# Performance work log

Hardware: AMD Instinct MI355X
Metric: run time of the kernel (lower is better)

## Reference

```python
import jax, jax.numpy as jnp
import numpy as np

EMBED = 1024
HEADS = 16
HD = EMBED // HEADS
SCALE_BASE = 512
OFFSET = 0

def _dup_interleave(m):
    # [T, half] -> [T, 2*half], each column repeated twice interleaved
    return jnp.repeat(m, 2, axis=-1)

def _rotate_every_two(x):
    x1 = x[..., ::2]
    x2 = x[..., 1::2]
    return jnp.stack([-x2, x1], axis=-1).reshape(x.shape)

def _xpos(x, offset, downscale):
    # x: [B, H, T, D]; torchscale XPOS
    T = x.shape[2]
    half = HD // 2
    scale_vec = (jnp.arange(0, HD, 2, dtype=jnp.float32) + 0.4 * HD) / (1.4 * HD)  # [half]
    min_pos = -(T + offset) // 2
    power = jnp.arange(min_pos, min_pos + T, dtype=jnp.float32) / SCALE_BASE  # [T]
    scale = scale_vec[None, :] ** power[:, None]  # [T, half]
    inv_freq = 1.0 / (10000.0 ** (jnp.arange(half, dtype=jnp.float32) / half))
    ang = jnp.arange(T, dtype=jnp.float32)[:, None] * inv_freq[None, :]  # [T, half]
    sin, cos = jnp.sin(ang), jnp.cos(ang)
    if downscale:
        scale = 1.0 / scale
    sin_s = _dup_interleave(sin * scale)  # [T, D]
    cos_s = _dup_interleave(cos * scale)  # [T, D]
    return x * cos_s + _rotate_every_two(x) * sin_s

def setup_inputs() -> dict:
    rng = jax.random.key(0)
    ks = jax.random.split(rng, 8)
    B, T, C = 2, 2048, EMBED
    s = 1.0 / np.sqrt(C)
    return {
        "query": jax.random.normal(ks[0], (B, T, C), jnp.float32),
        "key": jax.random.normal(ks[1], (B, T, C), jnp.float32),
        "value": jax.random.normal(ks[2], (B, T, C), jnp.float32),
        "key_padding_mask": jnp.zeros((B, T), jnp.bool_),
        "Wq": jax.random.normal(ks[3], (C, C), jnp.float32) * s,
        "bq": jnp.zeros((C,), jnp.float32),
        "Wk": jax.random.normal(ks[4], (C, C), jnp.float32) * s,
        "bk": jnp.zeros((C,), jnp.float32),
        "Wv": jax.random.normal(ks[5], (C, C), jnp.float32) * s,
        "bv": jnp.zeros((C,), jnp.float32),
        "Wo": jax.random.normal(ks[6], (C, C), jnp.float32) * s,
        "bo": jnp.zeros((C,), jnp.float32),
    }

def reference(query, key, value, key_padding_mask, Wq, bq, Wk, bk, Wv, bv, Wo, bo):
    B, T, C = query.shape
    def split(x):  # [B,T,C] -> [B,H,T,D]
        return x.reshape(B, T, HEADS, HD).transpose(0, 2, 1, 3)
    q = split(query @ Wq + bq)
    k = split(key @ Wk + bk)
    v = split(value @ Wv + bv)
    k = _xpos(k, 0, True)
    q = _xpos(q, OFFSET, False)
    scores = jnp.einsum('bhtd,bhsd->bhts', q * (HD ** -0.5), k)
    scores = jnp.where(key_padding_mask[:, None, None, :], -jnp.inf, scores)
    probs = jax.nn.softmax(scores.astype(jnp.float32), axis=-1).astype(scores.dtype)
    out = jnp.einsum('bhts,bhsd->bhtd', probs, v)
    out = out.transpose(0, 2, 1, 3).reshape(B, T, C)
    return out @ Wo + bo
```

## Files before the change

kernel.cpp:

```cpp
#include <hip/hip_runtime.h>
#include <math.h>


typedef _Float16 half4v __attribute__((ext_vector_type(4)));
typedef _Float16 half8v __attribute__((ext_vector_type(8)));
typedef float floatx4 __attribute__((ext_vector_type(4)));

#define GLOAD_LDS16(g, l)                                          \
    __builtin_amdgcn_global_load_lds(                              \
        (const __attribute__((address_space(1))) void*)(g),        \
        (__attribute__((address_space(3))) void*)(l), 16, 0, 0)

__global__ __launch_bounds__(256) void convert_x_kernel(
    const float* __restrict__ q, const float* __restrict__ k,
    const float* __restrict__ v, _Float16* __restrict__ oq,
    _Float16* __restrict__ ok, _Float16* __restrict__ ov)
{
    const int z = blockIdx.y;
    const float* src = (z == 0) ? q : (z == 1) ? k : v;
    _Float16* dst = (z == 0) ? oq : (z == 1) ? ok : ov;
    const size_t i = ((size_t)blockIdx.x * 256 + threadIdx.x) * 4;
    const float4 f = *(const float4*)(src + i);
    half4v h = {(_Float16)f.x, (_Float16)f.y, (_Float16)f.z, (_Float16)f.w};
    *(half4v*)(dst + i) = h;
}

__global__ __launch_bounds__(256) void convert_wt_kernel(
    const float* __restrict__ Wq, const float* __restrict__ Wk,
    const float* __restrict__ Wv, const float* __restrict__ Wo,
    _Float16* __restrict__ Wt)
{
    __shared__ float t[64][65];
    const int z = blockIdx.z;
    const float* W = (z == 0) ? Wq : (z == 1) ? Wk : (z == 2) ? Wv : Wo;
    _Float16* out = Wt + (size_t)z * 1048576;
    const int kt = blockIdx.y << 6;
    const int nb = blockIdx.x << 6;
    const int tid = threadIdx.x;

#pragma unroll
    for (int rep = 0; rep < 4; ++rep) {
        const int row = rep * 16 + (tid >> 4);
        const int col = (tid & 15) << 2;
        const float4 f = *(const float4*)(W + (size_t)(kt + row) * 1024 + nb + col);
        t[row][col + 0] = f.x; t[row][col + 1] = f.y;
        t[row][col + 2] = f.z; t[row][col + 3] = f.w;
    }
    __syncthreads();
#pragma unroll
    for (int rep = 0; rep < 2; ++rep) {
        const int n = rep * 32 + (tid >> 3);
        const int k8 = (tid & 7) << 3;
        half8v h;
#pragma unroll
        for (int j = 0; j < 8; ++j) h[j] = (_Float16)t[k8 + j][n];
        *(half8v*)(out + (size_t)(nb + n) * 1024 + kt + k8) = h;
    }
}

__global__ __launch_bounds__(256) void xpos_tables_kernel(
    float* __restrict__ csQ, float* __restrict__ snQ,
    float* __restrict__ csK, float* __restrict__ snK)
{
    const int idx = blockIdx.x * 256 + threadIdx.x;
    const int t = idx >> 5, j = idx & 31;
    const float invf = exp2f(-(float)j * 0.41524101186092029f);
    const float ang = (float)t * invf;
    const float sn = __sinf(ang), cs = __cosf(ang);
    const float lsv = log2f((2.0f * j + 25.6f) * (1.0f / 89.6f));
    const float pw = ((float)t - 1024.0f) * (1.0f / 512.0f);
    const float scQ = exp2f(pw * lsv) * 0.125f * 1.44269504088896341f;
    const float scK = exp2f(-pw * lsv);
    const int o = (t << 6) + 2 * j;
    csQ[o] = cs * scQ; csQ[o + 1] = cs * scQ;
    snQ[o] = -sn * scQ; snQ[o + 1] = sn * scQ;
    csK[o] = cs * scK; csK[o + 1] = cs * scK;
    snK[o] = -sn * scK; snK[o + 1] = sn * scK;
}

__global__ __launch_bounds__(256) void gemm_qkv_kernel(
    const _Float16* __restrict__ Xq, const _Float16* __restrict__ Xk,
    const _Float16* __restrict__ Xv, const _Float16* __restrict__ Wt,
    const float* __restrict__ bq, const float* __restrict__ bk,
    const float* __restrict__ bv,
    const float* __restrict__ csQ, const float* __restrict__ snQ,
    const float* __restrict__ csK, const float* __restrict__ snK,
    _Float16* __restrict__ Qr, _Float16* __restrict__ Kr,
    _Float16* __restrict__ Vt)
{
    __shared__ _Float16 smem[16384];

    const int zone  = blockIdx.x >> 3;
    const int ncol0 = (blockIdx.x & 7) << 7;
    const _Float16* Ab = (zone == 0) ? Xq : (zone == 1) ? Xk : Xv;
    const _Float16* Bb = Wt + (size_t)zone * 1048576;
    const float* bias = (zone == 0) ? bq : (zone == 1) ? bk : bv;

    const int tid  = threadIdx.x;
    const int wave = tid >> 6;
    const int lane = tid & 63;
    const int l15  = lane & 15;
    const int q4   = lane >> 4;

    const int mBase = blockIdx.y << 7;

    const int c0 = tid, c1 = tid + 256;
    const int rA0 = c0 >> 2, g0 = (c0 & 3) ^ ((rA0 >> 1) & 3);
    const int rA1 = c1 >> 2, g1 = (c1 & 3) ^ ((rA1 >> 1) & 3);
    const _Float16* gA0 = Ab + (size_t)(mBase + rA0) * 1024 + g0 * 8;
    const _Float16* gA1 = Ab + (size_t)(mBase + rA1) * 1024 + g1 * 8;
    const _Float16* gB0 = Bb + (size_t)(ncol0 + rA0) * 1024 + g0 * 8;
    const _Float16* gB1 = Bb + (size_t)(ncol0 + rA1) * 1024 + g1 * 8;

    const int mW = (wave >> 1) << 6;
    const int nW = (wave & 1) << 6;

    floatx4 acc[4][4];
#pragma unroll
    for (int i = 0; i < 4; ++i)
#pragma unroll
        for (int j = 0; j < 4; ++j) acc[i][j] = (floatx4){0.f, 0.f, 0.f, 0.f};

#define QKV_STAGE(k0, buf)                                         \
    do {                                                           \
        _Float16* sb = smem + (buf) * 8192;                        \
        GLOAD_LDS16(gA0 + (k0), sb + c0 * 8);                      \
        GLOAD_LDS16(gA1 + (k0), sb + c1 * 8);                      \
        GLOAD_LDS16(gB0 + (k0), sb + 4096 + c0 * 8);               \
        GLOAD_LDS16(gB1 + (k0), sb + 4096 + c1 * 8);               \
    } while (0)

    QKV_STAGE(0, 0);

    for (int it = 0; it < 32; ++it) {
        const int b = it & 1;
        __syncthreads();
        if (it < 31) QKV_STAGE((it + 1) << 5, b ^ 1);

        const _Float16* sb = smem + b * 8192;
        half8v af[4], bf[4];
#pragma unroll
        for (int mt = 0; mt < 4; ++mt) {
            const int r = mW + mt * 16 + l15;
            af[mt] = *(const half8v*)(sb + r * 32 + ((q4 ^ ((r >> 1) & 3)) << 3));
        }
#pragma unroll
        for (int nt = 0; nt < 4; ++nt) {
            const int r = nW + nt * 16 + l15;
            bf[nt] = *(const half8v*)(sb + 4096 + r * 32 + ((q4 ^ ((r >> 1) & 3)) << 3));
        }
#pragma unroll
        for (int mt = 0; mt < 4; ++mt)
#pragma unroll
            for (int nt = 0; nt < 4; ++nt)
                acc[mt][nt] = __builtin_amdgcn_mfma_f32_16x16x32_f16(
                    af[mt], bf[nt], acc[mt][nt], 0, 0, 0);
    }
#undef QKV_STAGE

    if (zone <= 1) {
        const float* csT = zone ? csK : csQ;
        const float* snT = zone ? snK : snQ;
        _Float16* dst = zone ? Kr : Qr;
#pragma unroll
        for (int nt = 0; nt < 4; ++nt) {
            const int col = ncol0 + nW + nt * 16 + l15;
            const int h = col >> 6, d = col & 63;
            const float bb = bias[col];
#pragma unroll
            for (int mt = 0; mt < 4; ++mt) {
#pragma unroll
                for (int reg = 0; reg < 4; ++reg) {
                    const int r = mBase + mW + mt * 16 + q4 * 4 + reg;
                    const int t = r & 2047, b = r >> 11;
                    const float x = acc[mt][nt][reg] + bb;
                    const float p = __shfl_xor(x, 1);
                    const int ti = (t << 6) + d;
                    const float o = csT[ti] * x + snT[ti] * p;
                    dst[(((size_t)(b * 16 + h) * 2048 + t) << 6) + d] = (_Float16)o;
                }
            }
        }
    } else {
#pragma unroll
        for (int nt = 0; nt < 4; ++nt) {
            const int col = ncol0 + nW + nt * 16 + l15;
            const int h = col >> 6, d = col & 63;
            const float bb = bias[col];
#pragma unroll
            for (int mt = 0; mt < 4; ++mt) {
                const int r0 = mBase + mW + mt * 16 + q4 * 4;
                const int t0 = r0 & 2047, b = r0 >> 11;
                half4v w = {(_Float16)(acc[mt][nt][0] + bb),
                            (_Float16)(acc[mt][nt][1] + bb),
                            (_Float16)(acc[mt][nt][2] + bb),
                            (_Float16)(acc[mt][nt][3] + bb)};
                *(half4v*)(Vt + ((size_t)(b * 16 + h) * 64 + d) * 2048 + t0) = w;
            }
        }
    }
}

__global__ __launch_bounds__(512) void gemm_out_kernel(
    const _Float16* __restrict__ Ar, const _Float16* __restrict__ Wt,
    const float* __restrict__ bo, float* __restrict__ Out)
{
    __shared__ _Float16 smem[16384];

    const _Float16* Bb = Wt + (size_t)3 * 1048576;
    const int tid  = threadIdx.x;
    const int wave = tid >> 6;
    const int lane = tid & 63;
    const int l15  = lane & 15;
    const int q4   = lane >> 4;

    const int mBase = blockIdx.y << 7;
    const int nBase = blockIdx.x << 7;

    const int rS = tid >> 2, gS = (tid & 3) ^ ((rS >> 1) & 3);
    const _Float16* gA = Ar + (size_t)(mBase + rS) * 1024 + gS * 8;
    const _Float16* gB = Bb + (size_t)(nBase + rS) * 1024 + gS * 8;

    const int mW = (wave >> 2) << 6;
    const int nW = (wave & 3) << 5;

    floatx4 acc[4][2];
#pragma unroll
    for (int i = 0; i < 4; ++i)
#pragma unroll
        for (int j = 0; j < 2; ++j) acc[i][j] = (floatx4){0.f, 0.f, 0.f, 0.f};

#define OUT_STAGE(k0, buf)                                         \
    do {                                                           \
        _Float16* sb = smem + (buf) * 8192;                        \
        GLOAD_LDS16(gA + (k0), sb + tid * 8);                      \
        GLOAD_LDS16(gB + (k0), sb + 4096 + tid * 8);               \
    } while (0)

    OUT_STAGE(0, 0);

    for (int it = 0; it < 32; ++it) {
        const int b = it & 1;
        __syncthreads();
        if (it < 31) OUT_STAGE((it + 1) << 5, b ^ 1);

        const _Float16* sb = smem + b * 8192;
        half8v af[4], bf[2];
#pragma unroll
        for (int mt = 0; mt < 4; ++mt) {
            const int r = mW + mt * 16 + l15;
            af[mt] = *(const half8v*)(sb + r * 32 + ((q4 ^ ((r >> 1) & 3)) << 3));
        }
#pragma unroll
        for (int nt = 0; nt < 2; ++nt) {
            const int r = nW + nt * 16 + l15;
            bf[nt] = *(const half8v*)(sb + 4096 + r * 32 + ((q4 ^ ((r >> 1) & 3)) << 3));
        }
#pragma unroll
        for (int mt = 0; mt < 4; ++mt)
#pragma unroll
            for (int nt = 0; nt < 2; ++nt)
                acc[mt][nt] = __builtin_amdgcn_mfma_f32_16x16x32_f16(
                    af[mt], bf[nt], acc[mt][nt], 0, 0, 0);
    }
#undef OUT_STAGE

#pragma unroll
    for (int nt = 0; nt < 2; ++nt) {
        const int col = nBase + nW + nt * 16 + l15;
        const float bb = bo[col];
#pragma unroll
        for (int mt = 0; mt < 4; ++mt) {
#pragma unroll
            for (int reg = 0; reg < 4; ++reg) {
                const int r = mBase + mW + mt * 16 + q4 * 4 + reg;
                Out[(size_t)r * 1024 + col] = acc[mt][nt][reg] + bb;
            }
        }
    }
}

__global__ __launch_bounds__(512, 4) void attn_mfma_kernel(
    const _Float16* __restrict__ Q, const _Float16* __restrict__ K,
    const _Float16* __restrict__ Vt, _Float16* __restrict__ Ar)
{
    __shared__ _Float16 Ks[2][4096];
    __shared__ _Float16 Vs[2][4096];
    __shared__ _Float16 Ps[8][1024];

    const int tid  = threadIdx.x;
    const int wave = tid >> 6;
    const int lane = tid & 63;
    const int l15  = lane & 15;
    const int q4   = lane >> 4;
    const int swz  = l15 & 7;

    const int bh    = blockIdx.y;
    const int qBase = blockIdx.x << 7;
    const _Float16* Qh = Q  + ((size_t)bh << 17);
    const _Float16* Kh = K  + ((size_t)bh << 17);
    const _Float16* Vh = Vt + ((size_t)bh << 17);

    const _Float16* qp =
        Qh + ((size_t)(qBase + wave * 16 + l15) << 6) + q4 * 8;
    const half8v qf0 = *(const half8v*)(qp);
    const half8v qf1 = *(const half8v*)(qp + 32);

    floatx4 O[4];
#pragma unroll
    for (int i = 0; i < 4; ++i) O[i] = (floatx4){0.f, 0.f, 0.f, 0.f};
    floatx4 l_acc = (floatx4){0.f, 0.f, 0.f, 0.f};
    float mneg = 64.0f;
    const half8v ones = {(_Float16)1, (_Float16)1, (_Float16)1, (_Float16)1,
                         (_Float16)1, (_Float16)1, (_Float16)1, (_Float16)1};

    const int sA = tid >> 3, gA = (tid & 7) ^ (sA & 7);

#define STAGE(S0, BUF)                                                        \
    do {                                                                      \
        GLOAD_LDS16(Kh + (size_t)((S0) + sA) * 64 + gA * 8, &Ks[BUF][tid * 8]);\
        GLOAD_LDS16(Vh + (size_t)sA * 2048 + (S0) + gA * 8, &Vs[BUF][tid * 8]);\
    } while (0)

    STAGE(0, 0);

    for (int ci = 0; ci < 32; ++ci) {
        const int b = ci & 1;
        __syncthreads();
        if (ci < 31) STAGE((ci + 1) << 6, b ^ 1);

        const floatx4 bias = (floatx4){mneg, mneg, mneg, mneg};
        floatx4 St[4];
        __builtin_amdgcn_s_setprio(1);
#pragma unroll
        for (int ti = 0; ti < 4; ++ti) {
            const _Float16* kb = &Ks[b][(ti * 16 + l15) << 6];
            const half8v kf0 = *(const half8v*)(kb + ((q4 ^ swz) << 3));
            const half8v kf1 = *(const half8v*)(kb + (((q4 ^ 4) ^ swz) << 3));
            floatx4 a = __builtin_amdgcn_mfma_f32_16x16x32_f16(
                kf0, qf0, bias, 0, 0, 0);
            St[ti] = __builtin_amdgcn_mfma_f32_16x16x32_f16(
                kf1, qf1, a, 0, 0, 0);
        }
        __builtin_amdgcn_s_setprio(0);

        float mx0 = fmaxf(fmaxf(St[0][0], St[0][1]), St[0][2]);
        float mx1 = fmaxf(fmaxf(St[0][3], St[1][0]), St[1][1]);
        float mx2 = fmaxf(fmaxf(St[1][2], St[1][3]), St[2][0]);
        float mx3 = fmaxf(fmaxf(St[2][1], St[2][2]), St[2][3]);
        float mx4 = fmaxf(fmaxf(St[3][0], St[3][1]), St[3][2]);
        float mx  = fmaxf(fmaxf(mx0, mx1), mx2);
        mx = fmaxf(fmaxf(mx, mx3), fmaxf(mx4, St[3][3]));

        if (__any(mx > 8.0f)) {
            mx = fmaxf(mx, __shfl_xor(mx, 16));
            mx = fmaxf(mx, __shfl_xor(mx, 32));
            const float dlt = fmaxf(mx, 0.0f);
            const float alpha = __builtin_amdgcn_exp2f(-dlt);
            mneg -= dlt;
#pragma unroll
            for (int ti = 0; ti < 4; ++ti)
#pragma unroll
                for (int reg = 0; reg < 4; ++reg) St[ti][reg] -= dlt;
            float ar[4];
#pragma unroll
            for (int reg = 0; reg < 4; ++reg)
                ar[reg] = __shfl(alpha, 20 * q4 + reg);
#pragma unroll
            for (int dt = 0; dt < 4; ++dt)
#pragma unroll
                for (int reg = 0; reg < 4; ++reg) O[dt][reg] *= ar[reg];
#pragma unroll
            for (int reg = 0; reg < 4; ++reg) l_acc[reg] *= ar[reg];
        }

#pragma unroll
        for (int ti = 0; ti < 4; ++ti)
#pragma unroll
            for (int reg = 0; reg < 4; ++reg)
                St[ti][reg] = __builtin_amdgcn_exp2f(St[ti][reg]);

        _Float16* pw = &Ps[wave][l15 << 6];
#pragma unroll
        for (int ti = 0; ti < 4; ++ti) {
            const int sg = 2 * ti + (q4 >> 1);
            half4v pv = {(_Float16)St[ti][0], (_Float16)St[ti][1],
                         (_Float16)St[ti][2], (_Float16)St[ti][3]};
            *(half4v*)(pw + ((sg ^ swz) << 3) + ((q4 & 1) << 2)) = pv;
        }

        const _Float16* pr = &Ps[wave][l15 << 6];
        const half8v pa0 = *(const half8v*)(pr + ((q4 ^ swz) << 3));
        const half8v pa1 = *(const half8v*)(pr + (((q4 ^ 4) ^ swz) << 3));
        __builtin_amdgcn_s_setprio(1);
        l_acc = __builtin_amdgcn_mfma_f32_16x16x32_f16(pa0, ones, l_acc, 0, 0, 0);
        l_acc = __builtin_amdgcn_mfma_f32_16x16x32_f16(pa1, ones, l_acc, 0, 0, 0);
#pragma unroll
        for (int dt = 0; dt < 4; ++dt) {
            const _Float16* vbp = &Vs[b][(dt * 16 + l15) << 6];
            const half8v vb0 = *(const half8v*)(vbp + ((q4 ^ swz) << 3));
            const half8v vb1 = *(const half8v*)(vbp + (((q4 ^ 4) ^ swz) << 3));
            O[dt] = __builtin_amdgcn_mfma_f32_16x16x32_f16(
                pa0, vb0, O[dt], 0, 0, 0);
            O[dt] = __builtin_amdgcn_mfma_f32_16x16x32_f16(
                pa1, vb1, O[dt], 0, 0, 0);
        }
        __builtin_amdgcn_s_setprio(0);
    }
#undef STAGE

    const int b_ = bh >> 4, h = bh & 15;
#pragma unroll
    for (int reg = 0; reg < 4; ++reg) {
        const float inv = 1.0f / l_acc[reg];
        const int t = qBase + wave * 16 + 4 * q4 + reg;
        _Float16* po = Ar + ((size_t)(b_ * 2048 + t)) * 1024 + h * 64 + l15;
#pragma unroll
        for (int dt = 0; dt < 4; ++dt)
            po[dt * 16] = (_Float16)(O[dt][reg] * inv);
    }
}

extern "C" void kernel_launch(void* const* d_in, const int* in_sizes, int n_in,
                              void* d_out, int out_size, void* d_ws, size_t ws_size,
                              hipStream_t stream) {
    const float* q  = (const float*)d_in[0];
    const float* k  = (const float*)d_in[1];
    const float* v  = (const float*)d_in[2];
    const float* Wq = (const float*)d_in[4];
    const float* bq = (const float*)d_in[5];
    const float* Wk = (const float*)d_in[6];
    const float* bk = (const float*)d_in[7];
    const float* Wv = (const float*)d_in[8];
    const float* bv = (const float*)d_in[9];
    const float* Wo = (const float*)d_in[10];
    const float* bo = (const float*)d_in[11];
    float* out = (float*)d_out;

    _Float16* Xqf = (_Float16*)d_ws;
    _Float16* Xkf = Xqf + (size_t)4194304;
    _Float16* Xvf = Xkf + (size_t)4194304;
    _Float16* Wt  = Xvf + (size_t)4194304;
    _Float16* Qr  = Wt  + (size_t)4194304;
    _Float16* Kr  = Qr  + (size_t)4194304;
    _Float16* Vt  = Kr  + (size_t)4194304;
    _Float16* Ar  = Vt  + (size_t)4194304;

    float* csQ = (float*)Ar;
    float* snQ = csQ + 131072;
    float* csK = snQ + 131072;
    float* snK = csK + 131072;

    dim3 blk(256, 1, 1);
    convert_x_kernel<<<dim3(4096, 3, 1), blk, 0, stream>>>(q, k, v, Xqf, Xkf, Xvf);
    convert_wt_kernel<<<dim3(16, 16, 4), blk, 0, stream>>>(Wq, Wk, Wv, Wo, Wt);
    xpos_tables_kernel<<<dim3(256, 1, 1), blk, 0, stream>>>(csQ, snQ, csK, snK);
    gemm_qkv_kernel<<<dim3(24, 32, 1), blk, 0, stream>>>(
        Xqf, Xkf, Xvf, Wt, bq, bk, bv, csQ, snQ, csK, snK, Qr, Kr, Vt);
    attn_mfma_kernel<<<dim3(16, 32, 1), dim3(512, 1, 1), 0, stream>>>(Qr, Kr, Vt, Ar);
    gemm_out_kernel<<<dim3(8, 32, 1), dim3(512, 1, 1), 0, stream>>>(Ar, Wt, bo, out);
}
```

Measured before the change: 246.1 us.

## Fuse prep kernels, XCD-aware block remap, smaller out-GEMM tiles, unroll attention loop

Merges the three preprocessing kernels (activation cast, weight transpose, xpos tables) into one launch to cut launch overhead. Remaps block indices in the QKV GEMM, attention and output GEMM so that blocks sharing operands land on the same XCD for better L2 reuse. The output GEMM tile shrinks from 128x128 to 128x64 to launch more blocks, which costs more reloads of A. The attention chunk loop is unrolled by two through a macro so the buffer index is a compile-time constant.

```diff
diff --git a/kernel.cpp b/kernel.cpp
--- a/kernel.cpp
+++ b/kernel.cpp
@@ -11,71 +11,70 @@
         (const __attribute__((address_space(1))) void*)(g),        \
         (__attribute__((address_space(3))) void*)(l), 16, 0, 0)
 
-__global__ __launch_bounds__(256) void convert_x_kernel(
+__global__ __launch_bounds__(256) void prep_kernel(
     const float* __restrict__ q, const float* __restrict__ k,
     const float* __restrict__ v, _Float16* __restrict__ oq,
-    _Float16* __restrict__ ok, _Float16* __restrict__ ov)
-{
-    const int z = blockIdx.y;
-    const float* src = (z == 0) ? q : (z == 1) ? k : v;
-    _Float16* dst = (z == 0) ? oq : (z == 1) ? ok : ov;
-    const size_t i = ((size_t)blockIdx.x * 256 + threadIdx.x) * 4;
-    const float4 f = *(const float4*)(src + i);
-    half4v h = {(_Float16)f.x, (_Float16)f.y, (_Float16)f.z, (_Float16)f.w};
-    *(half4v*)(dst + i) = h;
-}
-
-__global__ __launch_bounds__(256) void convert_wt_kernel(
+    _Float16* __restrict__ ok, _Float16* __restrict__ ov,
     const float* __restrict__ Wq, const float* __restrict__ Wk,
     const float* __restrict__ Wv, const float* __restrict__ Wo,
-    _Float16* __restrict__ Wt)
-{
-    __shared__ float t[64][65];
-    const int z = blockIdx.z;
-    const float* W = (z == 0) ? Wq : (z == 1) ? Wk : (z == 2) ? Wv : Wo;
-    _Float16* out = Wt + (size_t)z * 1048576;
-    const int kt = blockIdx.y << 6;
-    const int nb = blockIdx.x << 6;
-    const int tid = threadIdx.x;
-
-#pragma unroll
-    for (int rep = 0; rep < 4; ++rep) {
-        const int row = rep * 16 + (tid >> 4);
-        const int col = (tid & 15) << 2;
-        const float4 f = *(const float4*)(W + (size_t)(kt + row) * 1024 + nb + col);
-        t[row][col + 0] = f.x; t[row][col + 1] = f.y;
-        t[row][col + 2] = f.z; t[row][col + 3] = f.w;
-    }
-    __syncthreads();
-#pragma unroll
-    for (int rep = 0; rep < 2; ++rep) {
-        const int n = rep * 32 + (tid >> 3);
-        const int k8 = (tid & 7) << 3;
-        half8v h;
-#pragma unroll
-        for (int j = 0; j < 8; ++j) h[j] = (_Float16)t[k8 + j][n];
-        *(half8v*)(out + (size_t)(nb + n) * 1024 + kt + k8) = h;
-    }
-}
-
-__global__ __launch_bounds__(256) void xpos_tables_kernel(
+    _Float16* __restrict__ Wt,
     float* __restrict__ csQ, float* __restrict__ snQ,
     float* __restrict__ csK, float* __restrict__ snK)
 {
-    const int idx = blockIdx.x * 256 + threadIdx.x;
-    const int t = idx >> 5, j = idx & 31;
-    const float invf = exp2f(-(float)j * 0.41524101186092029f);
-    const float ang = (float)t * invf;
-    const float sn = __sinf(ang), cs = __cosf(ang);
-    const float lsv = log2f((2.0f * j + 25.6f) * (1.0f / 89.6f));
-    const float pw = ((float)t - 1024.0f) * (1.0f / 512.0f);
-    const float scQ = exp2f(pw * lsv) * 0.125f * 1.44269504088896341f;
-    const float scK = exp2f(-pw * lsv);
-    const int o = (t << 6) + 2 * j;
-    csQ[o] = cs * scQ; csQ[o + 1] = cs * scQ;
-    snQ[o] = -sn * scQ; snQ[o + 1] = sn * scQ;
-    csK[o] = cs * scK; csK[o + 1] = cs * scK;
-    snK[o] = -sn * scK; snK[o + 1] = sn * scK;
+    __shared__ float t[64][65];
+    const int blk = blockIdx.x;
+    const int tid = threadIdx.x;
+
+    if (blk < 12288) {
+        const int z = blk >> 12;
+        const int xb = blk & 4095;
+        const float* src = (z == 0) ? q : (z == 1) ? k : v;
+        _Float16* dst = (z == 0) ? oq : (z == 1) ? ok : ov;
+        const size_t i = ((size_t)xb * 256 + tid) * 4;
+        const float4 f = *(const float4*)(src + i);
+        half4v h = {(_Float16)f.x, (_Float16)f.y, (_Float16)f.z, (_Float16)f.w};
+        *(half4v*)(dst + i) = h;
+    } else if (blk < 13312) {
+        const int idx = blk - 12288;
+        const int z = idx >> 8;
+        const int kt = ((idx >> 4) & 15) << 6;
+        const int nb = (idx & 15) << 6;
+        const float* W = (z == 0) ? Wq : (z == 1) ? Wk : (z == 2) ? Wv : Wo;
+        _Float16* out = Wt + (size_t)z * 1048576;
+#pragma unroll
+        for (int rep = 0; rep < 4; ++rep) {
+            const int row = rep * 16 + (tid >> 4);
+            const int col = (tid & 15) << 2;
+            const float4 f = *(const float4*)(W + (size_t)(kt + row) * 1024 + nb + col);
+            t[row][col + 0] = f.x; t[row][col + 1] = f.y;
+            t[row][col + 2] = f.z; t[row][col + 3] = f.w;
+        }
+        __syncthreads();
+#pragma unroll
+        for (int rep = 0; rep < 2; ++rep) {
+            const int n = rep * 32 + (tid >> 3);
+            const int k8 = (tid & 7) << 3;
+            half8v h;
+#pragma unroll
+            for (int j = 0; j < 8; ++j) h[j] = (_Float16)t[k8 + j][n];
+            *(half8v*)(out + (size_t)(nb + n) * 1024 + kt + k8) = h;
+        }
+    } else {
+        const int idx = (blk - 13312) * 256 + tid;
+        const int tt = idx >> 5, j = idx & 31;
+        const float invf = exp2f(-(float)j * 0.41524101186092029f);
+        const float ang = (float)tt * invf;
+        const float sn = __sinf(ang), cs = __cosf(ang);
+        const float lsv = log2f((2.0f * j + 25.6f) * (1.0f / 89.6f));
+        const float pw = ((float)tt - 1024.0f) * (1.0f / 512.0f);
+        const float scQ = exp2f(pw * lsv) * 0.125f * 1.44269504088896341f;
+        const float scK = exp2f(-pw * lsv);
+        const int o = (tt << 6) + 2 * j;
+        csQ[o] = cs * scQ; csQ[o + 1] = cs * scQ;
+        snQ[o] = -sn * scQ; snQ[o + 1] = sn * scQ;
+        csK[o] = cs * scK; csK[o + 1] = cs * scK;
+        snK[o] = -sn * scK; snK[o + 1] = sn * scK;
+    }
 }
 
 __global__ __launch_bounds__(256) void gemm_qkv_kernel(
@@ -90,8 +89,13 @@
 {
     __shared__ _Float16 smem[16384];
 
-    const int zone  = blockIdx.x >> 3;
-    const int ncol0 = (blockIdx.x & 7) << 7;
+    const int L = blockIdx.x;
+    const int xcd = L & 7, kk = L >> 3;
+    const int g = xcd + ((kk >> 3) << 3);
+    const int zone  = g >> 5;
+    const int ncol0 = (kk & 7) << 7;
+    const int mBase = (g & 31) << 7;
+
     const _Float16* Ab = (zone == 0) ? Xq : (zone == 1) ? Xk : Xv;
     const _Float16* Bb = Wt + (size_t)zone * 1048576;
     const float* bias = (zone == 0) ? bq : (zone == 1) ? bk : bv;
@@ -101,8 +105,6 @@
     const int lane = tid & 63;
     const int l15  = lane & 15;
     const int q4   = lane >> 4;
-
-    const int mBase = blockIdx.y << 7;
 
     const int c0 = tid, c1 = tid + 256;
     const int rA0 = c0 >> 2, g0 = (c0 & 3) ^ ((rA0 >> 1) & 3);
@@ -205,7 +207,7 @@
     const _Float16* __restrict__ Ar, const _Float16* __restrict__ Wt,
     const float* __restrict__ bo, float* __restrict__ Out)
 {
-    __shared__ _Float16 smem[16384];
+    __shared__ _Float16 smem[12288];
 
     const _Float16* Bb = Wt + (size_t)3 * 1048576;
     const int tid  = threadIdx.x;
@@ -214,27 +216,29 @@
     const int l15  = lane & 15;
     const int q4   = lane >> 4;
 
-    const int mBase = blockIdx.y << 7;
-    const int nBase = blockIdx.x << 7;
-
-    const int rS = tid >> 2, gS = (tid & 3) ^ ((rS >> 1) & 3);
-    const _Float16* gA = Ar + (size_t)(mBase + rS) * 1024 + gS * 8;
-    const _Float16* gB = Bb + (size_t)(nBase + rS) * 1024 + gS * 8;
-
-    const int mW = (wave >> 2) << 6;
-    const int nW = (wave & 3) << 5;
-
-    floatx4 acc[4][2];
-#pragma unroll
-    for (int i = 0; i < 4; ++i)
+    const int L = blockIdx.x;
+    const int xcd = L & 7, kk = L >> 3;
+    const int mBase = (xcd + ((kk >> 4) << 3)) << 7;
+    const int nBase = (kk & 15) << 6;
+
+    const int rA = tid >> 2, gSA = (tid & 3) ^ ((rA >> 1) & 3);
+    const _Float16* gA = Ar + (size_t)(mBase + rA) * 1024 + gSA * 8;
+    const _Float16* gB = Bb + (size_t)(nBase + rA) * 1024 + gSA * 8;
+
+    const int mW = (wave >> 1) << 5;
+    const int nW = (wave & 1) << 5;
+
+    floatx4 acc[2][2];
+#pragma unroll
+    for (int i = 0; i < 2; ++i)
 #pragma unroll
         for (int j = 0; j < 2; ++j) acc[i][j] = (floatx4){0.f, 0.f, 0.f, 0.f};
 
 #define OUT_STAGE(k0, buf)                                         \
     do {                                                           \
-        _Float16* sb = smem + (buf) * 8192;                        \
+        _Float16* sb = smem + (buf) * 6144;                        \
         GLOAD_LDS16(gA + (k0), sb + tid * 8);                      \
-        GLOAD_LDS16(gB + (k0), sb + 4096 + tid * 8);               \
+        if (tid < 256) GLOAD_LDS16(gB + (k0), sb + 4096 + tid * 8);\
     } while (0)
 
     OUT_STAGE(0, 0);
@@ -244,10 +248,10 @@
         __syncthreads();
         if (it < 31) OUT_STAGE((it + 1) << 5, b ^ 1);
 
-        const _Float16* sb = smem + b * 8192;
-        half8v af[4], bf[2];
-#pragma unroll
-        for (int mt = 0; mt < 4; ++mt) {
+        const _Float16* sb = smem + b * 6144;
+        half8v af[2], bf[2];
+#pragma unroll
+        for (int mt = 0; mt < 2; ++mt) {
             const int r = mW + mt * 16 + l15;
             af[mt] = *(const half8v*)(sb + r * 32 + ((q4 ^ ((r >> 1) & 3)) << 3));
         }
@@ -257,7 +261,7 @@
             bf[nt] = *(const half8v*)(sb + 4096 + r * 32 + ((q4 ^ ((r >> 1) & 3)) << 3));
         }
 #pragma unroll
-        for (int mt = 0; mt < 4; ++mt)
+        for (int mt = 0; mt < 2; ++mt)
 #pragma unroll
             for (int nt = 0; nt < 2; ++nt)
                 acc[mt][nt] = __builtin_amdgcn_mfma_f32_16x16x32_f16(
@@ -270,7 +274,7 @@
         const int col = nBase + nW + nt * 16 + l15;
         const float bb = bo[col];
 #pragma unroll
-        for (int mt = 0; mt < 4; ++mt) {
+        for (int mt = 0; mt < 2; ++mt) {
 #pragma unroll
             for (int reg = 0; reg < 4; ++reg) {
                 const int r = mBase + mW + mt * 16 + q4 * 4 + reg;
@@ -295,8 +299,10 @@
     const int q4   = lane >> 4;
     const int swz  = l15 & 7;
 
-    const int bh    = blockIdx.y;
-    const int qBase = blockIdx.x << 7;
+    const int L = blockIdx.x;
+    const int xcd = L & 7, r_ = L >> 3;
+    const int bh = xcd + ((r_ >> 4) << 3);
+    const int qBase = (r_ & 15) << 7;
     const _Float16* Qh = Q  + ((size_t)bh << 17);
     const _Float16* Kh = K  + ((size_t)bh << 17);
     const _Float16* Vh = Vt + ((size_t)bh << 17);
@@ -322,91 +328,88 @@
         GLOAD_LDS16(Vh + (size_t)sA * 2048 + (S0) + gA * 8, &Vs[BUF][tid * 8]);\
     } while (0)
 
+#define CHUNK(CI, B, DO_PREF)                                                 \
+    do {                                                                      \
+        __syncthreads();                                                      \
+        if (DO_PREF) STAGE(((CI) + 1) << 6, (B) ^ 1);                         \
+        const floatx4 bias = (floatx4){mneg, mneg, mneg, mneg};               \
+        floatx4 St[4];                                                        \
+        __builtin_amdgcn_s_setprio(1);                                        \
+        _Pragma("unroll")                                                     \
+        for (int ti = 0; ti < 4; ++ti) {                                      \
+            const _Float16* kb = &Ks[B][(ti * 16 + l15) << 6];                \
+            const half8v kf0 = *(const half8v*)(kb + ((q4 ^ swz) << 3));      \
+            const half8v kf1 = *(const half8v*)(kb + (((q4 ^ 4) ^ swz) << 3));\
+            floatx4 a = __builtin_amdgcn_mfma_f32_16x16x32_f16(               \
+                kf0, qf0, bias, 0, 0, 0);                                     \
+            St[ti] = __builtin_amdgcn_mfma_f32_16x16x32_f16(                  \
+                kf1, qf1, a, 0, 0, 0);                                        \
+        }                                                                     \
+        __builtin_amdgcn_s_setprio(0);                                        \
+        float mx0 = fmaxf(fmaxf(St[0][0], St[0][1]), St[0][2]);               \
+        float mx1 = fmaxf(fmaxf(St[0][3], St[1][0]), St[1][1]);               \
+        float mx2 = fmaxf(fmaxf(St[1][2], St[1][3]), St[2][0]);               \
+        float mx3 = fmaxf(fmaxf(St[2][1], St[2][2]), St[2][3]);               \
+        float mx4 = fmaxf(fmaxf(St[3][0], St[3][1]), St[3][2]);               \
+        float mx  = fmaxf(fmaxf(mx0, mx1), mx2);                              \
+        mx = fmaxf(fmaxf(mx, mx3), fmaxf(mx4, St[3][3]));                     \
+        if (__any(mx > 8.0f)) {                                               \
+            mx = fmaxf(mx, __shfl_xor(mx, 16));                               \
+            mx = fmaxf(mx, __shfl_xor(mx, 32));                               \
+            const float dlt = fmaxf(mx, 0.0f);                                \
+            const float alpha = __builtin_amdgcn_exp2f(-dlt);                 \
+            mneg -= dlt;                                                      \
+            _Pragma("unroll")                                                 \
+            for (int ti = 0; ti < 4; ++ti)                                    \
+                for (int reg = 0; reg < 4; ++reg) St[ti][reg] -= dlt;         \
+            float ar[4];                                                      \
+            _Pragma("unroll")                                                 \
+            for (int reg = 0; reg < 4; ++reg)                                 \
+                ar[reg] = __shfl(alpha, 20 * q4 + reg);                       \
+            _Pragma("unroll")                                                 \
+            for (int dt = 0; dt < 4; ++dt)                                    \
+                for (int reg = 0; reg < 4; ++reg) O[dt][reg] *= ar[reg];      \
+            _Pragma("unroll")                                                 \
+            for (int reg = 0; reg < 4; ++reg) l_acc[reg] *= ar[reg];          \
+        }                                                                     \
+        _Pragma("unroll")                                                     \
+        for (int ti = 0; ti < 4; ++ti)                                        \
+            for (int reg = 0; reg < 4; ++reg)                                 \
+                St[ti][reg] = __builtin_amdgcn_exp2f(St[ti][reg]);            \
+        _Float16* pw = &Ps[wave][l15 << 6];                                   \
+        _Pragma("unroll")                                                     \
+        for (int ti = 0; ti < 4; ++ti) {                                      \
+            const int sg = 2 * ti + (q4 >> 1);                                \
+            half4v pv = {(_Float16)St[ti][0], (_Float16)St[ti][1],            \
+                         (_Float16)St[ti][2], (_Float16)St[ti][3]};           \
+            *(half4v*)(pw + ((sg ^ swz) << 3) + ((q4 & 1) << 2)) = pv;        \
+        }                                                                     \
+        const _Float16* pr = &Ps[wave][l15 << 6];                             \
+        const half8v pa0 = *(const half8v*)(pr + ((q4 ^ swz) << 3));          \
+        const half8v pa1 = *(const half8v*)(pr + (((q4 ^ 4) ^ swz) << 3));    \
+        __builtin_amdgcn_s_setprio(1);                                        \
+        l_acc = __builtin_amdgcn_mfma_f32_16x16x32_f16(pa0, ones, l_acc, 0, 0, 0); \
+        l_acc = __builtin_amdgcn_mfma_f32_16x16x32_f16(pa1, ones, l_acc, 0, 0, 0); \
+        _Pragma("unroll")                                                     \
+        for (int dt = 0; dt < 4; ++dt) {                                      \
+            const _Float16* vbp = &Vs[B][(dt * 16 + l15) << 6];               \
+            const half8v vb0 = *(const half8v*)(vbp + ((q4 ^ swz) << 3));     \
+            const half8v vb1 = *(const half8v*)(vbp + (((q4 ^ 4) ^ swz) << 3));\
+            O[dt] = __builtin_amdgcn_mfma_f32_16x16x32_f16(                   \
+                pa0, vb0, O[dt], 0, 0, 0);                                    \
+            O[dt] = __builtin_amdgcn_mfma_f32_16x16x32_f16(                   \
+                pa1, vb1, O[dt], 0, 0, 0);                                    \
+        }                                                                     \
+        __builtin_amdgcn_s_setprio(0);                                        \
+    } while (0)
+
     STAGE(0, 0);
 
-    for (int ci = 0; ci < 32; ++ci) {
-        const int b = ci & 1;
-        __syncthreads();
-        if (ci < 31) STAGE((ci + 1) << 6, b ^ 1);
-
-        const floatx4 bias = (floatx4){mneg, mneg, mneg, mneg};
-        floatx4 St[4];
-        __builtin_amdgcn_s_setprio(1);
-#pragma unroll
-        for (int ti = 0; ti < 4; ++ti) {
-            const _Float16* kb = &Ks[b][(ti * 16 + l15) << 6];
-            const half8v kf0 = *(const half8v*)(kb + ((q4 ^ swz) << 3));
-            const half8v kf1 = *(const half8v*)(kb + (((q4 ^ 4) ^ swz) << 3));
-            floatx4 a = __builtin_amdgcn_mfma_f32_16x16x32_f16(
-                kf0, qf0, bias, 0, 0, 0);
-            St[ti] = __builtin_amdgcn_mfma_f32_16x16x32_f16(
-                kf1, qf1, a, 0, 0, 0);
-        }
-        __builtin_amdgcn_s_setprio(0);
-
-        float mx0 = fmaxf(fmaxf(St[0][0], St[0][1]), St[0][2]);
-        float mx1 = fmaxf(fmaxf(St[0][3], St[1][0]), St[1][1]);
-        float mx2 = fmaxf(fmaxf(St[1][2], St[1][3]), St[2][0]);
-        float mx3 = fmaxf(fmaxf(St[2][1], St[2][2]), St[2][3]);
-        float mx4 = fmaxf(fmaxf(St[3][0], St[3][1]), St[3][2]);
-        float mx  = fmaxf(fmaxf(mx0, mx1), mx2);
-        mx = fmaxf(fmaxf(mx, mx3), fmaxf(mx4, St[3][3]));
-
-        if (__any(mx > 8.0f)) {
-            mx = fmaxf(mx, __shfl_xor(mx, 16));
-            mx = fmaxf(mx, __shfl_xor(mx, 32));
-            const float dlt = fmaxf(mx, 0.0f);
-            const float alpha = __builtin_amdgcn_exp2f(-dlt);
-            mneg -= dlt;
-#pragma unroll
-            for (int ti = 0; ti < 4; ++ti)
-#pragma unroll
-                for (int reg = 0; reg < 4; ++reg) St[ti][reg] -= dlt;
-            float ar[4];
-#pragma unroll
-            for (int reg = 0; reg < 4; ++reg)
-                ar[reg] = __shfl(alpha, 20 * q4 + reg);
-#pragma unroll
-            for (int dt = 0; dt < 4; ++dt)
-#pragma unroll
-                for (int reg = 0; reg < 4; ++reg) O[dt][reg] *= ar[reg];
-#pragma unroll
-            for (int reg = 0; reg < 4; ++reg) l_acc[reg] *= ar[reg];
-        }
-
-#pragma unroll
-        for (int ti = 0; ti < 4; ++ti)
-#pragma unroll
-            for (int reg = 0; reg < 4; ++reg)
-                St[ti][reg] = __builtin_amdgcn_exp2f(St[ti][reg]);
-
-        _Float16* pw = &Ps[wave][l15 << 6];
-#pragma unroll
-        for (int ti = 0; ti < 4; ++ti) {
-            const int sg = 2 * ti + (q4 >> 1);
-            half4v pv = {(_Float16)St[ti][0], (_Float16)St[ti][1],
-                         (_Float16)St[ti][2], (_Float16)St[ti][3]};
-            *(half4v*)(pw + ((sg ^ swz) << 3) + ((q4 & 1) << 2)) = pv;
-        }
-
-        const _Float16* pr = &Ps[wave][l15 << 6];
-        const half8v pa0 = *(const half8v*)(pr + ((q4 ^ swz) << 3));
-        const half8v pa1 = *(const half8v*)(pr + (((q4 ^ 4) ^ swz) << 3));
-        __builtin_amdgcn_s_setprio(1);
-        l_acc = __builtin_amdgcn_mfma_f32_16x16x32_f16(pa0, ones, l_acc, 0, 0, 0);
-        l_acc = __builtin_amdgcn_mfma_f32_16x16x32_f16(pa1, ones, l_acc, 0, 0, 0);
-#pragma unroll
-        for (int dt = 0; dt < 4; ++dt) {
-            const _Float16* vbp = &Vs[b][(dt * 16 + l15) << 6];
-            const half8v vb0 = *(const half8v*)(vbp + ((q4 ^ swz) << 3));
-            const half8v vb1 = *(const half8v*)(vbp + (((q4 ^ 4) ^ swz) << 3));
-            O[dt] = __builtin_amdgcn_mfma_f32_16x16x32_f16(
-                pa0, vb0, O[dt], 0, 0, 0);
-            O[dt] = __builtin_amdgcn_mfma_f32_16x16x32_f16(
-                pa1, vb1, O[dt], 0, 0, 0);
-        }
-        __builtin_amdgcn_s_setprio(0);
-    }
+    for (int ci = 0; ci < 32; ci += 2) {
+        CHUNK(ci, 0, true);
+        CHUNK(ci + 1, 1, (ci + 1) < 31);
+    }
+#undef CHUNK
 #undef STAGE
 
     const int b_ = bh >> 4, h = bh & 15;
@@ -451,12 +454,10 @@
     float* csK = snQ + 131072;
     float* snK = csK + 131072;
 
-    dim3 blk(256, 1, 1);
-    convert_x_kernel<<<dim3(4096, 3, 1), blk, 0, stream>>>(q, k, v, Xqf, Xkf, Xvf);
-    convert_wt_kernel<<<dim3(16, 16, 4), blk, 0, stream>>>(Wq, Wk, Wv, Wo, Wt);
-    xpos_tables_kernel<<<dim3(256, 1, 1), blk, 0, stream>>>(csQ, snQ, csK, snK);
-    gemm_qkv_kernel<<<dim3(24, 32, 1), blk, 0, stream>>>(
+    prep_kernel<<<dim3(13568, 1, 1), dim3(256, 1, 1), 0, stream>>>(
+        q, k, v, Xqf, Xkf, Xvf, Wq, Wk, Wv, Wo, Wt, csQ, snQ, csK, snK);
+    gemm_qkv_kernel<<<dim3(768, 1, 1), dim3(256, 1, 1), 0, stream>>>(
         Xqf, Xkf, Xvf, Wt, bq, bk, bv, csQ, snQ, csK, snK, Qr, Kr, Vt);
-    attn_mfma_kernel<<<dim3(16, 32, 1), dim3(512, 1, 1), 0, stream>>>(Qr, Kr, Vt, Ar);
-    gemm_out_kernel<<<dim3(8, 32, 1), dim3(512, 1, 1), 0, stream>>>(Ar, Wt, bo, out);
+    attn_mfma_kernel<<<dim3(512, 1, 1), dim3(512, 1, 1), 0, stream>>>(Qr, Kr, Vt, Ar);
+    gemm_out_kernel<<<dim3(512, 1, 1), dim3(512, 1, 1), 0, stream>>>(Ar, Wt, bo, out);
 }
```

After: 239.5 us. -2.7%, faster.
